# Performance work log

Measured on AMD Instinct MI355X. Metric: run time of the kernel, lower is better.

The kernel has to match this reference:

```python
import jax, jax.numpy as jnp
import numpy as np

COMMITMENT_COST = 0.25
DIST_SCALE = 400.0


def setup_inputs() -> dict:
    key = jax.random.key(0)
    ks = jax.random.split(key, 6)
    B, T, D, K = 64, 1024, 512, 512
    s = 1.0 / np.sqrt(D)
    return {
        "inputs": jax.random.normal(ks[0], (B, T, D), dtype=jnp.float32),
        "mean_W": jax.random.normal(ks[1], (D, D), dtype=jnp.float32) * s,
        "mean_b": jax.random.normal(ks[2], (D,), dtype=jnp.float32) * s,
        "logvar_W": jax.random.normal(ks[3], (D, K), dtype=jnp.float32) * s,
        "logvar_b": jax.random.normal(ks[4], (K,), dtype=jnp.float32) * s,
        "embedding": jax.random.normal(ks[5], (K, D), dtype=jnp.float32),
    }


def reference(inputs, mean_W, mean_b, logvar_W, logvar_b, embedding):
    sg = jax.lax.stop_gradient
    D = embedding.shape[1]
    flat = inputs.reshape(-1, D)                      # [N, D]
    x = flat @ mean_W + mean_b                        # mean_layer, [N, D]
    z_logvar = x @ logvar_W + logvar_b                # logvar_layer, [N, K]
    # squared euclidean distances to codebook, [N, K]
    distances = (
        jnp.sum(x * x, axis=1, keepdims=True)
        + jnp.sum(embedding * embedding, axis=1)
        - 2.0 * (x @ embedding.T)
    )
    smooth = jnp.exp(-2.0 * z_logvar)                 # 1/exp(logvar)^2
    d = distances / DIST_SCALE
    prob = jnp.exp(-d * (0.5 * smooth)) / jnp.sqrt(smooth)
    probs = prob / jnp.sum(prob, axis=1, keepdims=True)  # per-row normalize, [N, K]
    quantized = (probs @ embedding).reshape(inputs.shape)
    e_latent_loss = jnp.mean((sg(quantized) - inputs) ** 2)
    q_latent_loss = jnp.mean((quantized - sg(inputs)) ** 2)
    loss = q_latent_loss + COMMITMENT_COST * e_latent_loss
    quantized_st = inputs + sg(quantized - inputs)    # straight-through
    avg_probs = jnp.mean(probs, axis=0)
    perplexity = jnp.exp(-jnp.sum(avg_probs * jnp.log(avg_probs + 1e-10)))
    return loss, quantized_st, perplexity, probs
```

## Files before the change

kernel.cpp:

```cpp
#include <hip/hip_runtime.h>
#include <stdint.h>

#define BM 128
#define BN 128
#define BK 32
#define DIMD 512
#define NROWS 65536
#define QOFF 1
#define PERPOFF 33554433
#define PROBSOFF 33554434
#define NELEM 33554432

typedef __attribute__((ext_vector_type(8))) short bf16x8;
typedef __attribute__((ext_vector_type(4))) short s16x4;
typedef __attribute__((ext_vector_type(4))) float f32x4;

typedef const __attribute__((address_space(1))) void* gas_ptr;
typedef __attribute__((address_space(3))) void* las_ptr;

__device__ __forceinline__ short f2bf(float x){
  uint32_t u = __builtin_bit_cast(uint32_t, x);
  uint32_t r = (u + 0x7fffu + ((u >> 16) & 1u)) >> 16;
  return (short)(uint16_t)r;
}
__device__ __forceinline__ float bf2f(short h){
  return __builtin_bit_cast(float, ((uint32_t)(uint16_t)h) << 16);
}

__device__ __forceinline__ void stage_bf16(const short* __restrict__ g, int row0, int ld, int k0,
                                           short* lds){
  int tid = threadIdx.x;
#pragma unroll
  for (int i = 0; i < 2; ++i){
    int t = tid + i * 256;
    int row = t >> 2, c = t & 3;
    const short* src = g + (long)(row0 + row) * ld + k0 + c * 8;
    __builtin_amdgcn_global_load_lds((gas_ptr)src, (las_ptr)(lds + t * 8), 16, 0, 0);
  }
}

__device__ __forceinline__ void stage_f32_split(const float* __restrict__ g, int row0, int ld, int k0,
                                                short* hi, short* lo){
  int tid = threadIdx.x;
#pragma unroll
  for (int i = 0; i < 4; ++i){
    int t = tid + i * 256;
    int row = t >> 3, c = t & 7;
    const float4 v = *(const float4*)(g + (long)(row0 + row) * ld + k0 + c * 4);
    short h0 = f2bf(v.x), h1 = f2bf(v.y), h2 = f2bf(v.z), h3 = f2bf(v.w);
    s16x4 hv; hv[0] = h0; hv[1] = h1; hv[2] = h2; hv[3] = h3;
    s16x4 lv;
    lv[0] = f2bf(v.x - bf2f(h0)); lv[1] = f2bf(v.y - bf2f(h1));
    lv[2] = f2bf(v.z - bf2f(h2)); lv[3] = f2bf(v.w - bf2f(h3));
    *(s16x4*)(hi + row * BK + c * 4) = hv;
    *(s16x4*)(lo + row * BK + c * 4) = lv;
  }
}

__device__ __forceinline__ bf16x8 frag(const short* lds, int r, int q){
  return *(const bf16x8*)(lds + r * BK + q * 8);
}

__global__ __launch_bounds__(256) void k_convert_w(
    const float* __restrict__ meanW, const float* __restrict__ lvW, const float* __restrict__ emb,
    short* __restrict__ MWThi, short* __restrict__ MWTlo,
    short* __restrict__ VWh, short* __restrict__ VWl,
    short* __restrict__ E, short* __restrict__ ET, float* __restrict__ enorm)
{
  int b = blockIdx.x;
  int tid = threadIdx.x;
  float esum = 0.f;
  for (int j = tid; j < 512; j += 256){
    float w = meanW[b * 512 + j];
    short h = f2bf(w); short l = f2bf(w - bf2f(h));
    MWThi[j * 512 + b] = h; MWTlo[j * 512 + b] = l;
    float v = lvW[b * 512 + j];
    h = f2bf(v); l = f2bf(v - bf2f(h));
    long offW = ((long)(b >> 5) << 14) + j * 32 + (b & 31);
    VWh[offW] = h; VWl[offW] = l;
    float e = emb[b * 512 + j];
    short eh = f2bf(e);
    E[((long)(j >> 5) << 14) + b * 32 + (j & 31)] = eh;
    ET[((long)(b >> 5) << 14) + j * 32 + (b & 31)] = eh;
    esum += e * e;
  }
  for (int o = 32; o >= 1; o >>= 1) esum += __shfl_xor(esum, o);
  __shared__ float red[4];
  if ((tid & 63) == 0) red[tid >> 6] = esum;
  __syncthreads();
  if (tid == 0) enorm[b] = red[0] + red[1] + red[2] + red[3];
}

__global__ __launch_bounds__(256, 2) void k_gemm_mean(
    const float* __restrict__ inp, const short* __restrict__ Bhi, const short* __restrict__ Blo,
    const float* __restrict__ bias, short* __restrict__ Xhi, short* __restrict__ Xlo,
    float* __restrict__ xnorm)
{
  __shared__ short Ah[BM * BK], Al[BM * BK], Bh[BN * BK], Bl[BN * BK];
  int tid = threadIdx.x;
  int n0 = blockIdx.x * BM, c0 = blockIdx.y * BN;
  int lane = tid & 63, wid = tid >> 6;
  int wm = wid >> 1, wn = wid & 1;
  int q = lane >> 4, m = lane & 15;
  f32x4 acc[4][4];
#pragma unroll
  for (int i = 0; i < 4; i++)
#pragma unroll
    for (int j = 0; j < 4; j++)
#pragma unroll
      for (int r = 0; r < 4; r++) acc[i][j][r] = 0.f;

  for (int k0 = 0; k0 < DIMD; k0 += BK){
    __syncthreads();
    stage_f32_split(inp, n0, DIMD, k0, Ah, Al);
    stage_bf16(Bhi, c0, DIMD, k0, Bh);
    stage_bf16(Blo, c0, DIMD, k0, Bl);
    __syncthreads();
    bf16x8 ah[4], al[4], bh[4], bl[4];
#pragma unroll
    for (int i = 0; i < 4; i++){
      ah[i] = frag(Ah, wm * 64 + i * 16 + m, q);
      al[i] = frag(Al, wm * 64 + i * 16 + m, q);
      bh[i] = frag(Bh, wn * 64 + i * 16 + m, q);
      bl[i] = frag(Bl, wn * 64 + i * 16 + m, q);
    }
#pragma unroll
    for (int i = 0; i < 4; i++)
#pragma unroll
      for (int j = 0; j < 4; j++){
        acc[i][j] = __builtin_amdgcn_mfma_f32_16x16x32_bf16(ah[i], bh[j], acc[i][j], 0, 0, 0);
        acc[i][j] = __builtin_amdgcn_mfma_f32_16x16x32_bf16(ah[i], bl[j], acc[i][j], 0, 0, 0);
        acc[i][j] = __builtin_amdgcn_mfma_f32_16x16x32_bf16(al[i], bh[j], acc[i][j], 0, 0, 0);
      }
  }
#pragma unroll
  for (int i = 0; i < 4; i++){
#pragma unroll
    for (int r = 0; r < 4; r++){
      int row = n0 + wm * 64 + i * 16 + q * 4 + r;
      float xn = 0.f;
#pragma unroll
      for (int j = 0; j < 4; j++){
        int col = c0 + wn * 64 + j * 16 + m;
        float x = acc[i][j][r] + bias[col];
        short h = f2bf(x);
        short l = f2bf(x - bf2f(h));
        long off = ((long)(row >> 6) << 15) + ((long)(col >> 5) << 11) + (row & 63) * 32 + (col & 31);
        Xhi[off] = h;
        Xlo[off] = l;
        xn += x * x;
      }
      xn += __shfl_xor(xn, 1); xn += __shfl_xor(xn, 2);
      xn += __shfl_xor(xn, 4); xn += __shfl_xor(xn, 8);
      if (m == 0) atomicAdd(&xnorm[row], xn);
    }
  }
}

__global__ __launch_bounds__(1024) void k_fused(
    const short* __restrict__ Xh, const short* __restrict__ Xl,
    const short* __restrict__ Vh, const short* __restrict__ Vl,
    const short* __restrict__ Eb, const short* __restrict__ Et,
    const float* __restrict__ lvb, const float* __restrict__ xnorm,
    const float* __restrict__ enorm, const float* __restrict__ inp,
    float* __restrict__ probs, float* __restrict__ qout,
    float* __restrict__ Pacc, float* __restrict__ lossacc)
{
  __shared__ short P[64 * 512];
  __shared__ float rrM[16][64];
  __shared__ float rrS[16][64];

  const int tid = threadIdx.x;
  const int n0 = blockIdx.x * 64;
  const int lane = tid & 63, wid = tid >> 6;
  const int q = lane >> 4, m = lane & 15;
  const int c0 = wid * 32;

  const short* Xhb = Xh + (long)blockIdx.x * 32768;
  const short* Xlb = Xl + (long)blockIdx.x * 32768;

  f32x4 accZ[4][2];
#pragma unroll
  for (int i = 0; i < 4; i++)
#pragma unroll
    for (int j = 0; j < 2; j++)
#pragma unroll
      for (int r = 0; r < 4; r++) accZ[i][j][r] = 0.f;

  for (int ks = 0; ks < 16; ++ks){
    const short* xh = Xhb + ks * 2048;
    const short* xl = Xlb + ks * 2048;
    const short* vh = Vh + ks * 16384;
    const short* vl = Vl + ks * 16384;
    bf16x8 ah[4], al[4], bh[2], bl[2];
#pragma unroll
    for (int i = 0; i < 4; i++){
      ah[i] = *(const bf16x8*)(xh + i * 512 + m * 32 + q * 8);
      al[i] = *(const bf16x8*)(xl + i * 512 + m * 32 + q * 8);
    }
#pragma unroll
    for (int j = 0; j < 2; j++){
      bh[j] = *(const bf16x8*)(vh + (c0 + j * 16 + m) * 32 + q * 8);
      bl[j] = *(const bf16x8*)(vl + (c0 + j * 16 + m) * 32 + q * 8);
    }
#pragma unroll
    for (int j = 0; j < 2; j++)
#pragma unroll
      for (int i = 0; i < 4; i++){
        accZ[i][j] = __builtin_amdgcn_mfma_f32_16x16x32_bf16(ah[i], bh[j], accZ[i][j], 0, 0, 0);
        accZ[i][j] = __builtin_amdgcn_mfma_f32_16x16x32_bf16(ah[i], bl[j], accZ[i][j], 0, 0, 0);
        accZ[i][j] = __builtin_amdgcn_mfma_f32_16x16x32_bf16(al[i], bh[j], accZ[i][j], 0, 0, 0);
      }
  }

  f32x4 accS[4][2];
#pragma unroll
  for (int i = 0; i < 4; i++)
#pragma unroll
    for (int j = 0; j < 2; j++)
#pragma unroll
      for (int r = 0; r < 4; r++) accS[i][j][r] = 0.f;
  for (int ks = 0; ks < 16; ++ks){
    const short* xh = Xhb + ks * 2048;
    const short* eb = Eb + ks * 16384;
    bf16x8 ah[4], be[2];
#pragma unroll
    for (int i = 0; i < 4; i++) ah[i] = *(const bf16x8*)(xh + i * 512 + m * 32 + q * 8);
#pragma unroll
    for (int j = 0; j < 2; j++) be[j] = *(const bf16x8*)(eb + (c0 + j * 16 + m) * 32 + q * 8);
#pragma unroll
    for (int j = 0; j < 2; j++)
#pragma unroll
      for (int i = 0; i < 4; i++)
        accS[i][j] = __builtin_amdgcn_mfma_f32_16x16x32_bf16(ah[i], be[j], accS[i][j], 0, 0, 0);
  }

  float lvbv[2], env[2];
#pragma unroll
  for (int j = 0; j < 2; j++){
    int col = c0 + j * 16 + m;
    lvbv[j] = lvb[col];
    env[j] = enorm[col];
  }
  float xnv[4][4];
#pragma unroll
  for (int i = 0; i < 4; i++)
#pragma unroll
    for (int r = 0; r < 4; r++) xnv[i][r] = xnorm[n0 + i * 16 + q * 4 + r];

  const float inv800 = 0.5f / 400.0f;
#pragma unroll
  for (int i = 0; i < 4; i++)
#pragma unroll
    for (int j = 0; j < 2; j++)
#pragma unroll
      for (int r = 0; r < 4; r++){
        float z = accZ[i][j][r] + lvbv[j];
        float s = accS[i][j][r];
        float sm = __expf(-2.f * z);
        accS[i][j][r] = z - inv800 * (xnv[i][r] + env[j] - 2.f * s) * sm;
      }

#pragma unroll
  for (int i = 0; i < 4; i++)
#pragma unroll
    for (int r = 0; r < 4; r++){
      float v = fmaxf(accS[i][0][r], accS[i][1][r]);
      v = fmaxf(v, __shfl_xor(v, 1));
      v = fmaxf(v, __shfl_xor(v, 2));
      v = fmaxf(v, __shfl_xor(v, 4));
      v = fmaxf(v, __shfl_xor(v, 8));
      if (m == 0) rrM[wid][i * 16 + q * 4 + r] = v;
    }
  __syncthreads();
  float rmax;
  {
    float v = rrM[0][lane];
#pragma unroll
    for (int w = 1; w < 16; w++) v = fmaxf(v, rrM[w][lane]);
    rmax = v;
  }
  float mxf[4][4];
#pragma unroll
  for (int i = 0; i < 4; i++)
#pragma unroll
    for (int r = 0; r < 4; r++) mxf[i][r] = __shfl(rmax, i * 16 + q * 4 + r);

#pragma unroll
  for (int i = 0; i < 4; i++)
#pragma unroll
    for (int r = 0; r < 4; r++){
      float sacc = 0.f;
#pragma unroll
      for (int j = 0; j < 2; j++){
        float p = __expf(accS[i][j][r] - mxf[i][r]);
        accS[i][j][r] = p;
        sacc += p;
      }
      sacc += __shfl_xor(sacc, 1);
      sacc += __shfl_xor(sacc, 2);
      sacc += __shfl_xor(sacc, 4);
      sacc += __shfl_xor(sacc, 8);
      if (m == 0) rrS[wid][i * 16 + q * 4 + r] = sacc;
    }
  __syncthreads();
  float rsum;
  {
    float v = 0.f;
#pragma unroll
    for (int w = 0; w < 16; w++) v += rrS[w][lane];
    rsum = v;
  }
  float smr[4][4];
#pragma unroll
  for (int i = 0; i < 4; i++)
#pragma unroll
    for (int r = 0; r < 4; r++) smr[i][r] = __shfl(rsum, i * 16 + q * 4 + r);

  float pj[2];
  pj[0] = 0.f; pj[1] = 0.f;
#pragma unroll
  for (int i = 0; i < 4; i++)
#pragma unroll
    for (int r = 0; r < 4; r++){
      int rowl = i * 16 + q * 4 + r;
      long rowg = n0 + rowl;
      float inv = 1.0f / smr[i][r];
#pragma unroll
      for (int j = 0; j < 2; j++){
        int col = c0 + j * 16 + m;
        float qv = accS[i][j][r] * inv;
        probs[rowg * 512 + col] = qv;
        pj[j] += qv;
        int cg = col >> 3;
        P[rowl * 512 + (((cg ^ (rowl & 7)) << 3) | (col & 7))] = f2bf(qv);
      }
    }
#pragma unroll
  for (int j = 0; j < 2; j++){
    pj[j] += __shfl_xor(pj[j], 16);
    pj[j] += __shfl_xor(pj[j], 32);
  }
  if (lane < 16){
#pragma unroll
    for (int j = 0; j < 2; j++) atomicAdd(&Pacc[c0 + j * 16 + m], pj[j]);
  }
  __syncthreads();

  f32x4 accQ[4][2];
#pragma unroll
  for (int i = 0; i < 4; i++)
#pragma unroll
    for (int j = 0; j < 2; j++)
#pragma unroll
      for (int r = 0; r < 4; r++) accQ[i][j][r] = 0.f;
  for (int ks = 0; ks < 16; ++ks){
    int k0 = ks * 32;
    const short* et = Et + ks * 16384;
    bf16x8 pa[4], bq[2];
#pragma unroll
    for (int i = 0; i < 4; i++){
      int rowl = i * 16 + m;
      int cg = (k0 >> 3) + q;
      pa[i] = *(const bf16x8*)(P + rowl * 512 + ((cg ^ (rowl & 7)) << 3));
    }
#pragma unroll
    for (int j = 0; j < 2; j++) bq[j] = *(const bf16x8*)(et + (c0 + j * 16 + m) * 32 + q * 8);
#pragma unroll
    for (int j = 0; j < 2; j++)
#pragma unroll
      for (int i = 0; i < 4; i++)
        accQ[i][j] = __builtin_amdgcn_mfma_f32_16x16x32_bf16(pa[i], bq[j], accQ[i][j], 0, 0, 0);
  }

  float lsum = 0.f;
#pragma unroll
  for (int i = 0; i < 4; i++)
#pragma unroll
    for (int r = 0; r < 4; r++){
      long rowg = n0 + i * 16 + q * 4 + r;
#pragma unroll
      for (int j = 0; j < 2; j++){
        int col = c0 + j * 16 + m;
        float qv = accQ[i][j][r];
        long idx = rowg * 512 + col;
        qout[idx] = qv;
        float d = qv - inp[idx];
        lsum += d * d;
      }
    }
  lsum += __shfl_xor(lsum, 32);
  lsum += __shfl_xor(lsum, 16);
  lsum += __shfl_xor(lsum, 8);
  lsum += __shfl_xor(lsum, 4);
  lsum += __shfl_xor(lsum, 2);
  lsum += __shfl_xor(lsum, 1);
  if (lane == 0) rrM[0][wid] = lsum;
  __syncthreads();
  if (tid == 0){
    float t = 0.f;
#pragma unroll
    for (int w = 0; w < 16; w++) t += rrM[0][w];
    atomicAdd(lossacc, t);
  }
}

__global__ __launch_bounds__(256) void k_final(
    const float* __restrict__ Pacc, const float* __restrict__ lossacc, float* __restrict__ out)
{
  int tid = threadIdx.x;
  float h = 0.f;
  for (int k = tid; k < 512; k += 256){
    float a = Pacc[k] * (1.0f / 65536.0f);
    h += a * __logf(a + 1e-10f);
  }
  for (int o = 32; o >= 1; o >>= 1) h += __shfl_xor(h, o);
  __shared__ float red[4];
  if ((tid & 63) == 0) red[tid >> 6] = h;
  __syncthreads();
  if (tid == 0){
    float H = red[0] + red[1] + red[2] + red[3];
    out[0] = 1.25f * lossacc[0] * (1.0f / (float)NELEM);
    out[PERPOFF] = __expf(-H);
  }
}

extern "C" void kernel_launch(void* const* d_in, const int* in_sizes, int n_in,
                              void* d_out, int out_size, void* d_ws, size_t ws_size,
                              hipStream_t stream)
{
  const float* inp   = (const float*)d_in[0];
  const float* meanW = (const float*)d_in[1];
  const float* meanb = (const float*)d_in[2];
  const float* lvW   = (const float*)d_in[3];
  const float* lvb   = (const float*)d_in[4];
  const float* emb   = (const float*)d_in[5];
  float* out = (float*)d_out;

  char* w = (char*)d_ws;
  short* Xhi = (short*)w;   w += (size_t)NROWS * DIMD * 2;
  short* Xlo = (short*)w;   w += (size_t)NROWS * DIMD * 2;
  short* MWThi = (short*)w; w += 512 * 512 * 2;
  short* MWTlo = (short*)w; w += 512 * 512 * 2;
  short* VWh   = (short*)w; w += 512 * 512 * 2;
  short* VWl   = (short*)w; w += 512 * 512 * 2;
  short* E     = (short*)w; w += 512 * 512 * 2;
  short* ET    = (short*)w; w += 512 * 512 * 2;
  float* enorm = (float*)w; w += 512 * 4;
  float* stats = (float*)w;
  float* xnorm   = stats;
  float* Pacc    = stats + NROWS;
  float* lossacc = stats + NROWS + 512;

  hipMemsetAsync(stats, 0, (size_t)(NROWS + 512 + 16) * 4, stream);

  k_convert_w<<<512, 256, 0, stream>>>(meanW, lvW, emb, MWThi, MWTlo, VWh, VWl, E, ET, enorm);
  k_gemm_mean<<<dim3(512, 4), 256, 0, stream>>>(inp, MWThi, MWTlo, meanb, Xhi, Xlo, xnorm);
  k_fused<<<1024, 1024, 0, stream>>>(Xhi, Xlo, VWh, VWl, E, ET, lvb, xnorm, enorm, inp,
                                     out + PROBSOFF, out + QOFF, Pacc, lossacc);
  k_final<<<1, 256, 0, stream>>>(Pacc, lossacc, out);
}
```

Baseline: 870.4 us.

## Fuse mean-layer GEMM into main kernel, keeping x in LDS

Removes the separate mean-projection GEMM kernel and computes x = inputs@W+b inside the fused kernel. Each 64-row block loads its input rows, splits them into bf16 hi/lo in swizzled LDS, runs the split-precision GEMM, then overwrites LDS with x and computes row norms locally. This avoids writing and re-reading the 128 MB hi/lo x buffer in global memory, plus the xnorm atomics and memset. In exchange the fused kernel uses 128 KB of LDS per block and does more work per block. B-operand loads are now software-prefetched one k-step ahead.

New measurement: 699.7 us. 1.24x faster.

```diff
diff --git a/kernel.cpp b/kernel.cpp
--- a/kernel.cpp
+++ b/kernel.cpp
@@ -1,9 +1,6 @@
 #include <hip/hip_runtime.h>
 #include <stdint.h>
 
-#define BM 128
-#define BN 128
-#define BK 32
 #define DIMD 512
 #define NROWS 65536
 #define QOFF 1
@@ -15,9 +12,6 @@
 typedef __attribute__((ext_vector_type(4))) short s16x4;
 typedef __attribute__((ext_vector_type(4))) float f32x4;
 
-typedef const __attribute__((address_space(1))) void* gas_ptr;
-typedef __attribute__((address_space(3))) void* las_ptr;
-
 __device__ __forceinline__ short f2bf(float x){
   uint32_t u = __builtin_bit_cast(uint32_t, x);
   uint32_t r = (u + 0x7fffu + ((u >> 16) & 1u)) >> 16;
@@ -27,61 +21,31 @@
   return __builtin_bit_cast(float, ((uint32_t)(uint16_t)h) << 16);
 }
 
-__device__ __forceinline__ void stage_bf16(const short* __restrict__ g, int row0, int ld, int k0,
-                                           short* lds){
-  int tid = threadIdx.x;
-#pragma unroll
-  for (int i = 0; i < 2; ++i){
-    int t = tid + i * 256;
-    int row = t >> 2, c = t & 3;
-    const short* src = g + (long)(row0 + row) * ld + k0 + c * 8;
-    __builtin_amdgcn_global_load_lds((gas_ptr)src, (las_ptr)(lds + t * 8), 16, 0, 0);
-  }
-}
-
-__device__ __forceinline__ void stage_f32_split(const float* __restrict__ g, int row0, int ld, int k0,
-                                                short* hi, short* lo){
-  int tid = threadIdx.x;
-#pragma unroll
-  for (int i = 0; i < 4; ++i){
-    int t = tid + i * 256;
-    int row = t >> 3, c = t & 7;
-    const float4 v = *(const float4*)(g + (long)(row0 + row) * ld + k0 + c * 4);
-    short h0 = f2bf(v.x), h1 = f2bf(v.y), h2 = f2bf(v.z), h3 = f2bf(v.w);
-    s16x4 hv; hv[0] = h0; hv[1] = h1; hv[2] = h2; hv[3] = h3;
-    s16x4 lv;
-    lv[0] = f2bf(v.x - bf2f(h0)); lv[1] = f2bf(v.y - bf2f(h1));
-    lv[2] = f2bf(v.z - bf2f(h2)); lv[3] = f2bf(v.w - bf2f(h3));
-    *(s16x4*)(hi + row * BK + c * 4) = hv;
-    *(s16x4*)(lo + row * BK + c * 4) = lv;
-  }
-}
-
-__device__ __forceinline__ bf16x8 frag(const short* lds, int r, int q){
-  return *(const bf16x8*)(lds + r * BK + q * 8);
+__device__ __forceinline__ int aoff(int row, int kc){
+  return row * 512 + ((kc ^ (row & 7)) << 3);
 }
 
 __global__ __launch_bounds__(256) void k_convert_w(
     const float* __restrict__ meanW, const float* __restrict__ lvW, const float* __restrict__ emb,
-    short* __restrict__ MWThi, short* __restrict__ MWTlo,
+    short* __restrict__ MWfh, short* __restrict__ MWfl,
     short* __restrict__ VWh, short* __restrict__ VWl,
-    short* __restrict__ E, short* __restrict__ ET, float* __restrict__ enorm)
+    short* __restrict__ Eb, short* __restrict__ Et, float* __restrict__ enorm)
 {
   int b = blockIdx.x;
   int tid = threadIdx.x;
   float esum = 0.f;
   for (int j = tid; j < 512; j += 256){
+    long offB = ((long)(b >> 5) << 14) + j * 32 + (b & 31);
     float w = meanW[b * 512 + j];
     short h = f2bf(w); short l = f2bf(w - bf2f(h));
-    MWThi[j * 512 + b] = h; MWTlo[j * 512 + b] = l;
+    MWfh[offB] = h; MWfl[offB] = l;
     float v = lvW[b * 512 + j];
     h = f2bf(v); l = f2bf(v - bf2f(h));
-    long offW = ((long)(b >> 5) << 14) + j * 32 + (b & 31);
-    VWh[offW] = h; VWl[offW] = l;
+    VWh[offB] = h; VWl[offB] = l;
     float e = emb[b * 512 + j];
     short eh = f2bf(e);
-    E[((long)(j >> 5) << 14) + b * 32 + (j & 31)] = eh;
-    ET[((long)(b >> 5) << 14) + j * 32 + (b & 31)] = eh;
+    Eb[((long)(j >> 5) << 14) + b * 32 + (j & 31)] = eh;
+    Et[offB] = eh;
     esum += e * e;
   }
   for (int o = 32; o >= 1; o >>= 1) esum += __shfl_xor(esum, o);
@@ -91,82 +55,18 @@
   if (tid == 0) enorm[b] = red[0] + red[1] + red[2] + red[3];
 }
 
-__global__ __launch_bounds__(256, 2) void k_gemm_mean(
-    const float* __restrict__ inp, const short* __restrict__ Bhi, const short* __restrict__ Blo,
-    const float* __restrict__ bias, short* __restrict__ Xhi, short* __restrict__ Xlo,
-    float* __restrict__ xnorm)
-{
-  __shared__ short Ah[BM * BK], Al[BM * BK], Bh[BN * BK], Bl[BN * BK];
-  int tid = threadIdx.x;
-  int n0 = blockIdx.x * BM, c0 = blockIdx.y * BN;
-  int lane = tid & 63, wid = tid >> 6;
-  int wm = wid >> 1, wn = wid & 1;
-  int q = lane >> 4, m = lane & 15;
-  f32x4 acc[4][4];
-#pragma unroll
-  for (int i = 0; i < 4; i++)
-#pragma unroll
-    for (int j = 0; j < 4; j++)
-#pragma unroll
-      for (int r = 0; r < 4; r++) acc[i][j][r] = 0.f;
-
-  for (int k0 = 0; k0 < DIMD; k0 += BK){
-    __syncthreads();
-    stage_f32_split(inp, n0, DIMD, k0, Ah, Al);
-    stage_bf16(Bhi, c0, DIMD, k0, Bh);
-    stage_bf16(Blo, c0, DIMD, k0, Bl);
-    __syncthreads();
-    bf16x8 ah[4], al[4], bh[4], bl[4];
-#pragma unroll
-    for (int i = 0; i < 4; i++){
-      ah[i] = frag(Ah, wm * 64 + i * 16 + m, q);
-      al[i] = frag(Al, wm * 64 + i * 16 + m, q);
-      bh[i] = frag(Bh, wn * 64 + i * 16 + m, q);
-      bl[i] = frag(Bl, wn * 64 + i * 16 + m, q);
-    }
-#pragma unroll
-    for (int i = 0; i < 4; i++)
-#pragma unroll
-      for (int j = 0; j < 4; j++){
-        acc[i][j] = __builtin_amdgcn_mfma_f32_16x16x32_bf16(ah[i], bh[j], acc[i][j], 0, 0, 0);
-        acc[i][j] = __builtin_amdgcn_mfma_f32_16x16x32_bf16(ah[i], bl[j], acc[i][j], 0, 0, 0);
-        acc[i][j] = __builtin_amdgcn_mfma_f32_16x16x32_bf16(al[i], bh[j], acc[i][j], 0, 0, 0);
-      }
-  }
-#pragma unroll
-  for (int i = 0; i < 4; i++){
-#pragma unroll
-    for (int r = 0; r < 4; r++){
-      int row = n0 + wm * 64 + i * 16 + q * 4 + r;
-      float xn = 0.f;
-#pragma unroll
-      for (int j = 0; j < 4; j++){
-        int col = c0 + wn * 64 + j * 16 + m;
-        float x = acc[i][j][r] + bias[col];
-        short h = f2bf(x);
-        short l = f2bf(x - bf2f(h));
-        long off = ((long)(row >> 6) << 15) + ((long)(col >> 5) << 11) + (row & 63) * 32 + (col & 31);
-        Xhi[off] = h;
-        Xlo[off] = l;
-        xn += x * x;
-      }
-      xn += __shfl_xor(xn, 1); xn += __shfl_xor(xn, 2);
-      xn += __shfl_xor(xn, 4); xn += __shfl_xor(xn, 8);
-      if (m == 0) atomicAdd(&xnorm[row], xn);
-    }
-  }
-}
-
-__global__ __launch_bounds__(1024) void k_fused(
-    const short* __restrict__ Xh, const short* __restrict__ Xl,
-    const short* __restrict__ Vh, const short* __restrict__ Vl,
+__global__ __launch_bounds__(1024, 1) void k_fused(
+    const float* __restrict__ inp,
+    const short* __restrict__ MWfh, const short* __restrict__ MWfl,
+    const short* __restrict__ VWh, const short* __restrict__ VWl,
     const short* __restrict__ Eb, const short* __restrict__ Et,
-    const float* __restrict__ lvb, const float* __restrict__ xnorm,
-    const float* __restrict__ enorm, const float* __restrict__ inp,
+    const float* __restrict__ meanb, const float* __restrict__ lvb,
+    const float* __restrict__ enorm,
     float* __restrict__ probs, float* __restrict__ qout,
     float* __restrict__ Pacc, float* __restrict__ lossacc)
 {
-  __shared__ short P[64 * 512];
+  __shared__ short Ih[64 * 512];
+  __shared__ short Il[64 * 512];
   __shared__ float rrM[16][64];
   __shared__ float rrS[16][64];
 
@@ -176,8 +76,104 @@
   const int q = lane >> 4, m = lane & 15;
   const int c0 = wid * 32;
 
-  const short* Xhb = Xh + (long)blockIdx.x * 32768;
-  const short* Xlb = Xl + (long)blockIdx.x * 32768;
+  int boff0 = (c0 + m) * 32 + q * 8;
+  int boff1 = (c0 + 16 + m) * 32 + q * 8;
+
+  {
+    const float* inpb = inp + (long)n0 * 512;
+#pragma unroll
+    for (int it = 0; it < 8; ++it){
+      int fid = tid + it * 1024;
+      int row = fid >> 7, f = fid & 127;
+      const float4 v = *(const float4*)(inpb + (long)fid * 4);
+      short h0 = f2bf(v.x), h1 = f2bf(v.y), h2 = f2bf(v.z), h3 = f2bf(v.w);
+      s16x4 hv; hv[0] = h0; hv[1] = h1; hv[2] = h2; hv[3] = h3;
+      s16x4 lv;
+      lv[0] = f2bf(v.x - bf2f(h0)); lv[1] = f2bf(v.y - bf2f(h1));
+      lv[2] = f2bf(v.z - bf2f(h2)); lv[3] = f2bf(v.w - bf2f(h3));
+      int ch = (f >> 1) ^ (row & 7);
+      int addr = row * 512 + (ch << 3) + (f & 1) * 4;
+      *(s16x4*)(Ih + addr) = hv;
+      *(s16x4*)(Il + addr) = lv;
+    }
+  }
+  __syncthreads();
+
+  f32x4 accM[4][2];
+#pragma unroll
+  for (int i = 0; i < 4; i++)
+#pragma unroll
+    for (int j = 0; j < 2; j++)
+#pragma unroll
+      for (int r = 0; r < 4; r++) accM[i][j][r] = 0.f;
+  {
+    bf16x8 nbh0 = *(const bf16x8*)(MWfh + boff0);
+    bf16x8 nbh1 = *(const bf16x8*)(MWfh + boff1);
+    bf16x8 nbl0 = *(const bf16x8*)(MWfl + boff0);
+    bf16x8 nbl1 = *(const bf16x8*)(MWfl + boff1);
+#pragma unroll 2
+    for (int ks = 0; ks < 16; ++ks){
+      bf16x8 bh0 = nbh0, bh1 = nbh1, bl0 = nbl0, bl1 = nbl1;
+      if (ks < 15){
+        int o = (ks + 1) * 16384;
+        nbh0 = *(const bf16x8*)(MWfh + o + boff0);
+        nbh1 = *(const bf16x8*)(MWfh + o + boff1);
+        nbl0 = *(const bf16x8*)(MWfl + o + boff0);
+        nbl1 = *(const bf16x8*)(MWfl + o + boff1);
+      }
+      bf16x8 ah[4], al[4];
+#pragma unroll
+      for (int i = 0; i < 4; i++){
+        int off = aoff(i * 16 + m, ks * 4 + q);
+        ah[i] = *(const bf16x8*)(Ih + off);
+        al[i] = *(const bf16x8*)(Il + off);
+      }
+#pragma unroll
+      for (int i = 0; i < 4; i++){
+        accM[i][0] = __builtin_amdgcn_mfma_f32_16x16x32_bf16(ah[i], bh0, accM[i][0], 0, 0, 0);
+        accM[i][0] = __builtin_amdgcn_mfma_f32_16x16x32_bf16(ah[i], bl0, accM[i][0], 0, 0, 0);
+        accM[i][0] = __builtin_amdgcn_mfma_f32_16x16x32_bf16(al[i], bh0, accM[i][0], 0, 0, 0);
+        accM[i][1] = __builtin_amdgcn_mfma_f32_16x16x32_bf16(ah[i], bh1, accM[i][1], 0, 0, 0);
+        accM[i][1] = __builtin_amdgcn_mfma_f32_16x16x32_bf16(ah[i], bl1, accM[i][1], 0, 0, 0);
+        accM[i][1] = __builtin_amdgcn_mfma_f32_16x16x32_bf16(al[i], bh1, accM[i][1], 0, 0, 0);
+      }
+    }
+  }
+  __syncthreads();
+
+  {
+    float b0 = meanb[c0 + m], b1 = meanb[c0 + 16 + m];
+#pragma unroll
+    for (int i = 0; i < 4; i++)
+#pragma unroll
+      for (int r = 0; r < 4; r++){
+        int row = i * 16 + q * 4 + r;
+        float x0 = accM[i][0][r] + b0;
+        float x1 = accM[i][1][r] + b1;
+        int col0 = c0 + m, col1 = c0 + 16 + m;
+        short h0 = f2bf(x0), h1 = f2bf(x1);
+        int a0 = row * 512 + ((((col0 >> 3) ^ (row & 7)) << 3) | (col0 & 7));
+        int a1 = row * 512 + ((((col1 >> 3) ^ (row & 7)) << 3) | (col1 & 7));
+        Ih[a0] = h0; Il[a0] = f2bf(x0 - bf2f(h0));
+        Ih[a1] = h1; Il[a1] = f2bf(x1 - bf2f(h1));
+        float xn = x0 * x0 + x1 * x1;
+        xn += __shfl_xor(xn, 1); xn += __shfl_xor(xn, 2);
+        xn += __shfl_xor(xn, 4); xn += __shfl_xor(xn, 8);
+        if (m == 0) rrS[wid][row] = xn;
+      }
+  }
+  __syncthreads();
+
+  float xnv[4][4];
+  {
+    float v = 0.f;
+#pragma unroll
+    for (int w = 0; w < 16; w++) v += rrS[w][lane];
+#pragma unroll
+    for (int i = 0; i < 4; i++)
+#pragma unroll
+      for (int r = 0; r < 4; r++) xnv[i][r] = __shfl(v, i * 16 + q * 4 + r);
+  }
 
   f32x4 accZ[4][2];
 #pragma unroll
@@ -186,80 +182,85 @@
     for (int j = 0; j < 2; j++)
 #pragma unroll
       for (int r = 0; r < 4; r++) accZ[i][j][r] = 0.f;
-
-  for (int ks = 0; ks < 16; ++ks){
-    const short* xh = Xhb + ks * 2048;
-    const short* xl = Xlb + ks * 2048;
-    const short* vh = Vh + ks * 16384;
-    const short* vl = Vl + ks * 16384;
-    bf16x8 ah[4], al[4], bh[2], bl[2];
-#pragma unroll
-    for (int i = 0; i < 4; i++){
-      ah[i] = *(const bf16x8*)(xh + i * 512 + m * 32 + q * 8);
-      al[i] = *(const bf16x8*)(xl + i * 512 + m * 32 + q * 8);
-    }
-#pragma unroll
-    for (int j = 0; j < 2; j++){
-      bh[j] = *(const bf16x8*)(vh + (c0 + j * 16 + m) * 32 + q * 8);
-      bl[j] = *(const bf16x8*)(vl + (c0 + j * 16 + m) * 32 + q * 8);
-    }
+  {
+    bf16x8 nbh0 = *(const bf16x8*)(VWh + boff0);
+    bf16x8 nbh1 = *(const bf16x8*)(VWh + boff1);
+    bf16x8 nbl0 = *(const bf16x8*)(VWl + boff0);
+    bf16x8 nbl1 = *(const bf16x8*)(VWl + boff1);
+#pragma unroll 2
+    for (int ks = 0; ks < 16; ++ks){
+      bf16x8 bh0 = nbh0, bh1 = nbh1, bl0 = nbl0, bl1 = nbl1;
+      if (ks < 15){
+        int o = (ks + 1) * 16384;
+        nbh0 = *(const bf16x8*)(VWh + o + boff0);
+        nbh1 = *(const bf16x8*)(VWh + o + boff1);
+        nbl0 = *(const bf16x8*)(VWl + o + boff0);
+        nbl1 = *(const bf16x8*)(VWl + o + boff1);
+      }
+      bf16x8 ah[4], al[4];
+#pragma unroll
+      for (int i = 0; i < 4; i++){
+        int off = aoff(i * 16 + m, ks * 4 + q);
+        ah[i] = *(const bf16x8*)(Ih + off);
+        al[i] = *(const bf16x8*)(Il + off);
+      }
+#pragma unroll
+      for (int i = 0; i < 4; i++){
+        accZ[i][0] = __builtin_amdgcn_mfma_f32_16x16x32_bf16(ah[i], bh0, accZ[i][0], 0, 0, 0);
+        accZ[i][0] = __builtin_amdgcn_mfma_f32_16x16x32_bf16(ah[i], bl0, accZ[i][0], 0, 0, 0);
+        accZ[i][0] = __builtin_amdgcn_mfma_f32_16x16x32_bf16(al[i], bh0, accZ[i][0], 0, 0, 0);
+        accZ[i][1] = __builtin_amdgcn_mfma_f32_16x16x32_bf16(ah[i], bh1, accZ[i][1], 0, 0, 0);
+        accZ[i][1] = __builtin_amdgcn_mfma_f32_16x16x32_bf16(ah[i], bl1, accZ[i][1], 0, 0, 0);
+        accZ[i][1] = __builtin_amdgcn_mfma_f32_16x16x32_bf16(al[i], bh1, accZ[i][1], 0, 0, 0);
+      }
+    }
+  }
+
+  f32x4 accS[4][2];
+#pragma unroll
+  for (int i = 0; i < 4; i++)
 #pragma unroll
     for (int j = 0; j < 2; j++)
 #pragma unroll
-      for (int i = 0; i < 4; i++){
-        accZ[i][j] = __builtin_amdgcn_mfma_f32_16x16x32_bf16(ah[i], bh[j], accZ[i][j], 0, 0, 0);
-        accZ[i][j] = __builtin_amdgcn_mfma_f32_16x16x32_bf16(ah[i], bl[j], accZ[i][j], 0, 0, 0);
-        accZ[i][j] = __builtin_amdgcn_mfma_f32_16x16x32_bf16(al[i], bh[j], accZ[i][j], 0, 0, 0);
-      }
-  }
-
-  f32x4 accS[4][2];
-#pragma unroll
-  for (int i = 0; i < 4; i++)
-#pragma unroll
-    for (int j = 0; j < 2; j++)
-#pragma unroll
       for (int r = 0; r < 4; r++) accS[i][j][r] = 0.f;
-  for (int ks = 0; ks < 16; ++ks){
-    const short* xh = Xhb + ks * 2048;
-    const short* eb = Eb + ks * 16384;
-    bf16x8 ah[4], be[2];
-#pragma unroll
-    for (int i = 0; i < 4; i++) ah[i] = *(const bf16x8*)(xh + i * 512 + m * 32 + q * 8);
-#pragma unroll
-    for (int j = 0; j < 2; j++) be[j] = *(const bf16x8*)(eb + (c0 + j * 16 + m) * 32 + q * 8);
-#pragma unroll
-    for (int j = 0; j < 2; j++)
+  {
+    bf16x8 nb0 = *(const bf16x8*)(Eb + boff0);
+    bf16x8 nb1 = *(const bf16x8*)(Eb + boff1);
+#pragma unroll 2
+    for (int ks = 0; ks < 16; ++ks){
+      bf16x8 b0 = nb0, b1 = nb1;
+      if (ks < 15){
+        int o = (ks + 1) * 16384;
+        nb0 = *(const bf16x8*)(Eb + o + boff0);
+        nb1 = *(const bf16x8*)(Eb + o + boff1);
+      }
+      bf16x8 ah[4];
 #pragma unroll
       for (int i = 0; i < 4; i++)
-        accS[i][j] = __builtin_amdgcn_mfma_f32_16x16x32_bf16(ah[i], be[j], accS[i][j], 0, 0, 0);
-  }
-
-  float lvbv[2], env[2];
-#pragma unroll
-  for (int j = 0; j < 2; j++){
-    int col = c0 + j * 16 + m;
-    lvbv[j] = lvb[col];
-    env[j] = enorm[col];
-  }
-  float xnv[4][4];
-#pragma unroll
-  for (int i = 0; i < 4; i++)
-#pragma unroll
-    for (int r = 0; r < 4; r++) xnv[i][r] = xnorm[n0 + i * 16 + q * 4 + r];
-
-  const float inv800 = 0.5f / 400.0f;
-#pragma unroll
-  for (int i = 0; i < 4; i++)
-#pragma unroll
-    for (int j = 0; j < 2; j++)
+        ah[i] = *(const bf16x8*)(Ih + aoff(i * 16 + m, ks * 4 + q));
+#pragma unroll
+      for (int i = 0; i < 4; i++){
+        accS[i][0] = __builtin_amdgcn_mfma_f32_16x16x32_bf16(ah[i], b0, accS[i][0], 0, 0, 0);
+        accS[i][1] = __builtin_amdgcn_mfma_f32_16x16x32_bf16(ah[i], b1, accS[i][1], 0, 0, 0);
+      }
+    }
+  }
+
+  {
+    float lvb0 = lvb[c0 + m], lvb1 = lvb[c0 + 16 + m];
+    float en0 = enorm[c0 + m], en1 = enorm[c0 + 16 + m];
+    const float inv800 = 0.5f / 400.0f;
+#pragma unroll
+    for (int i = 0; i < 4; i++)
 #pragma unroll
       for (int r = 0; r < 4; r++){
-        float z = accZ[i][j][r] + lvbv[j];
-        float s = accS[i][j][r];
-        float sm = __expf(-2.f * z);
-        accS[i][j][r] = z - inv800 * (xnv[i][r] + env[j] - 2.f * s) * sm;
-      }
+        float z0 = accZ[i][0][r] + lvb0;
+        float z1 = accZ[i][1][r] + lvb1;
+        float sm0 = __expf(-2.f * z0), sm1 = __expf(-2.f * z1);
+        accS[i][0][r] = z0 - inv800 * (xnv[i][r] + en0 - 2.f * accS[i][0][r]) * sm0;
+        accS[i][1][r] = z1 - inv800 * (xnv[i][r] + en1 - 2.f * accS[i][1][r]) * sm1;
+      }
+  }
 
 #pragma unroll
   for (int i = 0; i < 4; i++)
@@ -273,30 +274,25 @@
       if (m == 0) rrM[wid][i * 16 + q * 4 + r] = v;
     }
   __syncthreads();
-  float rmax;
+  float mxf[4][4];
   {
     float v = rrM[0][lane];
 #pragma unroll
     for (int w = 1; w < 16; w++) v = fmaxf(v, rrM[w][lane]);
-    rmax = v;
-  }
-  float mxf[4][4];
-#pragma unroll
-  for (int i = 0; i < 4; i++)
-#pragma unroll
-    for (int r = 0; r < 4; r++) mxf[i][r] = __shfl(rmax, i * 16 + q * 4 + r);
+#pragma unroll
+    for (int i = 0; i < 4; i++)
+#pragma unroll
+      for (int r = 0; r < 4; r++) mxf[i][r] = __shfl(v, i * 16 + q * 4 + r);
+  }
 
 #pragma unroll
   for (int i = 0; i < 4; i++)
 #pragma unroll
     for (int r = 0; r < 4; r++){
-      float sacc = 0.f;
-#pragma unroll
-      for (int j = 0; j < 2; j++){
-        float p = __expf(accS[i][j][r] - mxf[i][r]);
-        accS[i][j][r] = p;
-        sacc += p;
-      }
+      float p0 = __expf(accS[i][0][r] - mxf[i][r]);
+      float p1 = __expf(accS[i][1][r] - mxf[i][r]);
+      accS[i][0][r] = p0; accS[i][1][r] = p1;
+      float sacc = p0 + p1;
       sacc += __shfl_xor(sacc, 1);
       sacc += __shfl_xor(sacc, 2);
       sacc += __shfl_xor(sacc, 4);
@@ -304,46 +300,43 @@
       if (m == 0) rrS[wid][i * 16 + q * 4 + r] = sacc;
     }
   __syncthreads();
-  float rsum;
+  float smr[4][4];
   {
     float v = 0.f;
 #pragma unroll
     for (int w = 0; w < 16; w++) v += rrS[w][lane];
-    rsum = v;
-  }
-  float smr[4][4];
-#pragma unroll
-  for (int i = 0; i < 4; i++)
-#pragma unroll
-    for (int r = 0; r < 4; r++) smr[i][r] = __shfl(rsum, i * 16 + q * 4 + r);
-
-  float pj[2];
-  pj[0] = 0.f; pj[1] = 0.f;
-#pragma unroll
-  for (int i = 0; i < 4; i++)
-#pragma unroll
-    for (int r = 0; r < 4; r++){
-      int rowl = i * 16 + q * 4 + r;
-      long rowg = n0 + rowl;
-      float inv = 1.0f / smr[i][r];
-#pragma unroll
-      for (int j = 0; j < 2; j++){
-        int col = c0 + j * 16 + m;
-        float qv = accS[i][j][r] * inv;
-        probs[rowg * 512 + col] = qv;
-        pj[j] += qv;
-        int cg = col >> 3;
-        P[rowl * 512 + (((cg ^ (rowl & 7)) << 3) | (col & 7))] = f2bf(qv);
-      }
-    }
-#pragma unroll
-  for (int j = 0; j < 2; j++){
-    pj[j] += __shfl_xor(pj[j], 16);
-    pj[j] += __shfl_xor(pj[j], 32);
-  }
-  if (lane < 16){
-#pragma unroll
-    for (int j = 0; j < 2; j++) atomicAdd(&Pacc[c0 + j * 16 + m], pj[j]);
+#pragma unroll
+    for (int i = 0; i < 4; i++)
+#pragma unroll
+      for (int r = 0; r < 4; r++) smr[i][r] = __shfl(v, i * 16 + q * 4 + r);
+  }
+
+  {
+    float pj0 = 0.f, pj1 = 0.f;
+#pragma unroll
+    for (int i = 0; i < 4; i++)
+#pragma unroll
+      for (int r = 0; r < 4; r++){
+        int row = i * 16 + q * 4 + r;
+        long rowg = n0 + row;
+        float inv = 1.0f / smr[i][r];
+        float q0 = accS[i][0][r] * inv;
+        float q1 = accS[i][1][r] * inv;
+        int col0 = c0 + m, col1 = c0 + 16 + m;
+        probs[rowg * 512 + col0] = q0;
+        probs[rowg * 512 + col1] = q1;
+        pj0 += q0; pj1 += q1;
+        int a0 = row * 512 + ((((col0 >> 3) ^ (row & 7)) << 3) | (col0 & 7));
+        int a1 = row * 512 + ((((col1 >> 3) ^ (row & 7)) << 3) | (col1 & 7));
+        Ih[a0] = f2bf(q0);
+        Ih[a1] = f2bf(q1);
+      }
+    pj0 += __shfl_xor(pj0, 16); pj0 += __shfl_xor(pj0, 32);
+    pj1 += __shfl_xor(pj1, 16); pj1 += __shfl_xor(pj1, 32);
+    if (lane < 16){
+      atomicAdd(&Pacc[c0 + m], pj0);
+      atomicAdd(&Pacc[c0 + 16 + m], pj1);
+    }
   }
   __syncthreads();
 
@@ -354,48 +347,52 @@
     for (int j = 0; j < 2; j++)
 #pragma unroll
       for (int r = 0; r < 4; r++) accQ[i][j][r] = 0.f;
-  for (int ks = 0; ks < 16; ++ks){
-    int k0 = ks * 32;
-    const short* et = Et + ks * 16384;
-    bf16x8 pa[4], bq[2];
-#pragma unroll
-    for (int i = 0; i < 4; i++){
-      int rowl = i * 16 + m;
-      int cg = (k0 >> 3) + q;
-      pa[i] = *(const bf16x8*)(P + rowl * 512 + ((cg ^ (rowl & 7)) << 3));
-    }
-#pragma unroll
-    for (int j = 0; j < 2; j++) bq[j] = *(const bf16x8*)(et + (c0 + j * 16 + m) * 32 + q * 8);
-#pragma unroll
-    for (int j = 0; j < 2; j++)
+  {
+    bf16x8 nb0 = *(const bf16x8*)(Et + boff0);
+    bf16x8 nb1 = *(const bf16x8*)(Et + boff1);
+#pragma unroll 2
+    for (int ks = 0; ks < 16; ++ks){
+      bf16x8 b0 = nb0, b1 = nb1;
+      if (ks < 15){
+        int o = (ks + 1) * 16384;
+        nb0 = *(const bf16x8*)(Et + o + boff0);
+        nb1 = *(const bf16x8*)(Et + o + boff1);
+      }
+      bf16x8 pa[4];
 #pragma unroll
       for (int i = 0; i < 4; i++)
-        accQ[i][j] = __builtin_amdgcn_mfma_f32_16x16x32_bf16(pa[i], bq[j], accQ[i][j], 0, 0, 0);
-  }
-
-  float lsum = 0.f;
-#pragma unroll
-  for (int i = 0; i < 4; i++)
-#pragma unroll
-    for (int r = 0; r < 4; r++){
-      long rowg = n0 + i * 16 + q * 4 + r;
-#pragma unroll
-      for (int j = 0; j < 2; j++){
-        int col = c0 + j * 16 + m;
-        float qv = accQ[i][j][r];
-        long idx = rowg * 512 + col;
-        qout[idx] = qv;
-        float d = qv - inp[idx];
-        lsum += d * d;
-      }
-    }
-  lsum += __shfl_xor(lsum, 32);
-  lsum += __shfl_xor(lsum, 16);
-  lsum += __shfl_xor(lsum, 8);
-  lsum += __shfl_xor(lsum, 4);
-  lsum += __shfl_xor(lsum, 2);
-  lsum += __shfl_xor(lsum, 1);
-  if (lane == 0) rrM[0][wid] = lsum;
+        pa[i] = *(const bf16x8*)(Ih + aoff(i * 16 + m, ks * 4 + q));
+#pragma unroll
+      for (int i = 0; i < 4; i++){
+        accQ[i][0] = __builtin_amdgcn_mfma_f32_16x16x32_bf16(pa[i], b0, accQ[i][0], 0, 0, 0);
+        accQ[i][1] = __builtin_amdgcn_mfma_f32_16x16x32_bf16(pa[i], b1, accQ[i][1], 0, 0, 0);
+      }
+    }
+  }
+
+  {
+    float lsum = 0.f;
+#pragma unroll
+    for (int i = 0; i < 4; i++)
+#pragma unroll
+      for (int r = 0; r < 4; r++){
+        long rowg = n0 + i * 16 + q * 4 + r;
+        float q0 = accQ[i][0][r], q1 = accQ[i][1][r];
+        long i0 = rowg * 512 + c0 + m;
+        long i1 = rowg * 512 + c0 + 16 + m;
+        qout[i0] = q0;
+        qout[i1] = q1;
+        float d0 = q0 - inp[i0], d1 = q1 - inp[i1];
+        lsum += d0 * d0 + d1 * d1;
+      }
+    lsum += __shfl_xor(lsum, 32);
+    lsum += __shfl_xor(lsum, 16);
+    lsum += __shfl_xor(lsum, 8);
+    lsum += __shfl_xor(lsum, 4);
+    lsum += __shfl_xor(lsum, 2);
+    lsum += __shfl_xor(lsum, 1);
+    if (lane == 0) rrM[0][wid] = lsum;
+  }
   __syncthreads();
   if (tid == 0){
     float t = 0.f;
@@ -438,25 +435,21 @@
   float* out = (float*)d_out;
 
   char* w = (char*)d_ws;
-  short* Xhi = (short*)w;   w += (size_t)NROWS * DIMD * 2;
-  short* Xlo = (short*)w;   w += (size_t)NROWS * DIMD * 2;
-  short* MWThi = (short*)w; w += 512 * 512 * 2;
-  short* MWTlo = (short*)w; w += 512 * 512 * 2;
-  short* VWh   = (short*)w; w += 512 * 512 * 2;
-  short* VWl   = (short*)w; w += 512 * 512 * 2;
-  short* E     = (short*)w; w += 512 * 512 * 2;
-  short* ET    = (short*)w; w += 512 * 512 * 2;
+  short* MWfh = (short*)w; w += 512 * 512 * 2;
+  short* MWfl = (short*)w; w += 512 * 512 * 2;
+  short* VWh  = (short*)w; w += 512 * 512 * 2;
+  short* VWl  = (short*)w; w += 512 * 512 * 2;
+  short* Eb   = (short*)w; w += 512 * 512 * 2;
+  short* Et   = (short*)w; w += 512 * 512 * 2;
   float* enorm = (float*)w; w += 512 * 4;
   float* stats = (float*)w;
-  float* xnorm   = stats;
-  float* Pacc    = stats + NROWS;
-  float* lossacc = stats + NROWS + 512;
-
-  hipMemsetAsync(stats, 0, (size_t)(NROWS + 512 + 16) * 4, stream);
-
-  k_convert_w<<<512, 256, 0, stream>>>(meanW, lvW, emb, MWThi, MWTlo, VWh, VWl, E, ET, enorm);
-  k_gemm_mean<<<dim3(512, 4), 256, 0, stream>>>(inp, MWThi, MWTlo, meanb, Xhi, Xlo, xnorm);
-  k_fused<<<1024, 1024, 0, stream>>>(Xhi, Xlo, VWh, VWl, E, ET, lvb, xnorm, enorm, inp,
+  float* Pacc    = stats;
+  float* lossacc = stats + 512;
+
+  hipMemsetAsync(stats, 0, (size_t)(512 + 16) * 4, stream);
+
+  k_convert_w<<<512, 256, 0, stream>>>(meanW, lvW, emb, MWfh, MWfl, VWh, VWl, Eb, Et, enorm);
+  k_fused<<<1024, 1024, 0, stream>>>(inp, MWfh, MWfl, VWh, VWl, Eb, Et, meanb, lvb, enorm,
                                      out + PROBSOFF, out + QOFF, Pacc, lossacc);
   k_final<<<1, 256, 0, stream>>>(Pacc, lossacc, out);
 }
```
